# Kernel tuning notes

Measured on AMD Instinct MI355X. Metric: run time of the kernel, lower is better.

Reference implementation:

```python
import jax, jax.numpy as jnp
import numpy as np

PI_2 = 3.14159 / 2  # matches the torch module's pi_2 constant
EPS = 1e-8          # F.cosine_similarity default eps


def setup_inputs() -> dict:
    key = jax.random.key(0)
    k1, k2 = jax.random.split(key)
    B, N, C, H, W = 32, 2000, 512, 7, 7
    key_t = jax.random.normal(k1, (B, C, H, W), dtype=jnp.float32)
    memory = jax.random.normal(k2, (N, C, H, W), dtype=jnp.float32)
    return {"key": key_t, "memory": memory}


def reference(key, memory):
    # Memory.read(key): cosine-similarity addressing + tan warp + softmax, then weighted read.
    B = key.shape[0]
    N = memory.shape[0]
    k = key.reshape(B, -1)        # [B, D], D = C*H*W
    m = memory.reshape(N, -1)     # [N, D]
    # cosine similarity with torch's eps clamping on norms
    dots = jnp.einsum('bd,nd->bn', k, m)                                   # [B, N]
    k_norm = jnp.maximum(jnp.sqrt(jnp.sum(k * k, axis=-1, keepdims=True)), EPS)  # [B, 1]
    m_norm = jnp.maximum(jnp.sqrt(jnp.sum(m * m, axis=-1)), EPS)                 # [N]
    cos = dots / (k_norm * m_norm[None, :])                                 # [B, N]
    w = jax.nn.softmax(jnp.tan(cos * PI_2), axis=1)                         # [B, N]
    # weighted read: sum_n w[b,n] * memory[n,c,h,w] -> [B, C, H, W]
    out = jnp.einsum('bn,nchw->bchw', w, memory)
    return out
```

## Files before the change

### kernel.cpp

```cpp
#include <hip/hip_runtime.h>
#include <math.h>

#define D_ELEMS 25088
#define D4      6272
#define N_MEM   2000
#define B_KEYS  32
#define PI_2F   1.570795f
#define EPSF    1e-8f
#define NSLICE  49
#define KSLICE  512
#define KSTEPS  16
#define NWAVES  (125 * NSLICE)
#define RTILE   100

using short8 = __attribute__((ext_vector_type(8))) short;
using short4v = __attribute__((ext_vector_type(4))) short;
using f32x4  = __attribute__((ext_vector_type(4))) float;


__device__ inline short f2bf(float x) {
    union { float f; unsigned u; } v; v.f = x;
    unsigned r = v.u + 0x7fffu + ((v.u >> 16) & 1u);
    return (short)(r >> 16);
}

__global__ __launch_bounds__(256) void k_prep(const float* __restrict__ key,
                                              short* __restrict__ keyb) {
    const int i = blockIdx.x * 256 + threadIdx.x;
    const float4 f = ((const float4*)key)[i];
    short4v s; s[0] = f2bf(f.x); s[1] = f2bf(f.y); s[2] = f2bf(f.z); s[3] = f2bf(f.w);
    ((short4v*)keyb)[i] = s;
}

__global__ __launch_bounds__(256) void k_dots_mfma(const short* __restrict__ keyb,
                                                  const float* __restrict__ mem,
                                                  float* __restrict__ dots_part,
                                                  float* __restrict__ mn2_part) {
    const int wid = blockIdx.x * 4 + (threadIdx.x >> 6);
    if (wid >= NWAVES) return;
    const int nt   = wid / NSLICE;
    const int s    = wid % NSLICE;
    const int n0   = nt * 16;
    const int lane = threadIdx.x & 63;
    const int quad = lane >> 4;
    const int l16  = lane & 15;
    const int k0   = s * KSLICE + quad * 8;

    const short* a0p = keyb + (size_t)l16 * D_ELEMS + k0;
    const short* a1p = keyb + (size_t)(16 + l16) * D_ELEMS + k0;
    const float4* bp = (const float4*)(mem + (size_t)(n0 + l16) * D_ELEMS + k0);

    f32x4 acc0 = {0.f, 0.f, 0.f, 0.f};
    f32x4 acc1 = {0.f, 0.f, 0.f, 0.f};
    float msq = 0.f;

    short8 a0 = *(const short8*)a0p;
    short8 a1 = *(const short8*)a1p;
    float4 f0 = bp[0], f1 = bp[1];

    for (int t = 0; t < KSTEPS; ++t) {
        const short8 a0c = a0, a1c = a1;
        const float4 f0c = f0, f1c = f1;
        if (t + 1 < KSTEPS) {
            a0 = *(const short8*)(a0p + (t + 1) * 32);
            a1 = *(const short8*)(a1p + (t + 1) * 32);
            f0 = bp[(t + 1) * 8];
            f1 = bp[(t + 1) * 8 + 1];
        }
        msq += f0c.x * f0c.x + f0c.y * f0c.y + f0c.z * f0c.z + f0c.w * f0c.w
             + f1c.x * f1c.x + f1c.y * f1c.y + f1c.z * f1c.z + f1c.w * f1c.w;
        short8 b;
        b[0] = f2bf(f0c.x); b[1] = f2bf(f0c.y); b[2] = f2bf(f0c.z); b[3] = f2bf(f0c.w);
        b[4] = f2bf(f1c.x); b[5] = f2bf(f1c.y); b[6] = f2bf(f1c.z); b[7] = f2bf(f1c.w);
        acc0 = __builtin_amdgcn_mfma_f32_16x16x32_bf16(a0c, b, acc0, 0, 0, 0);
        acc1 = __builtin_amdgcn_mfma_f32_16x16x32_bf16(a1c, b, acc1, 0, 0, 0);
    }

    float* dp = dots_part + (size_t)(s * N_MEM + n0 + l16) * B_KEYS;
#pragma unroll
    for (int r = 0; r < 4; ++r) {
        dp[quad * 4 + r]      = acc0[r];
        dp[16 + quad * 4 + r] = acc1[r];
    }

    msq += __shfl_xor(msq, 16, 64);
    msq += __shfl_xor(msq, 32, 64);
    if (lane < 16) mn2_part[s * N_MEM + n0 + lane] = msq;
}

__global__ __launch_bounds__(256) void k_reduce(const float* __restrict__ dots_part,
                                                const float* __restrict__ mn2_part,
                                                float* __restrict__ dots,
                                                float* __restrict__ mn2) {
    const int gid = blockIdx.x * 256 + threadIdx.x;
    float ds = 0.f;
#pragma unroll
    for (int s = 0; s < NSLICE; ++s) ds += dots_part[s * (N_MEM * B_KEYS) + gid];
    dots[gid] = ds;
    if (gid < N_MEM) {
        float ms = 0.f;
#pragma unroll
        for (int s = 0; s < NSLICE; ++s) ms += mn2_part[s * N_MEM + gid];
        mn2[gid] = ms;
    }
}

__global__ __launch_bounds__(512) void k_softmax(const float* __restrict__ key,
                                                 const float* __restrict__ dots,
                                                 const float* __restrict__ mn2,
                                                 float* __restrict__ w) {
    const int b   = blockIdx.x;
    const int tid = threadIdx.x;
    __shared__ float sred[512];
    __shared__ float xbuf[N_MEM];

    const float4* K4 = (const float4*)(key + (size_t)b * D_ELEMS);
    float ks = 0.f;
    for (int i = tid; i < D4; i += 512) {
        const float4 kf = K4[i];
        ks += kf.x * kf.x + kf.y * kf.y + kf.z * kf.z + kf.w * kf.w;
    }
    sred[tid] = ks;
    __syncthreads();
    for (int o = 256; o; o >>= 1) {
        if (tid < o) sred[tid] += sred[tid + o];
        __syncthreads();
    }
    const float knorm = fmaxf(sqrtf(sred[0]), EPSF);
    __syncthreads();

    float mx = -1e30f;
    for (int n = tid; n < N_MEM; n += 512) {
        const float mn = fmaxf(sqrtf(mn2[n]), EPSF);
        const float x  = __tanf((dots[n * B_KEYS + b] / (knorm * mn)) * PI_2F);
        xbuf[n] = x;
        mx = fmaxf(mx, x);
    }
    sred[tid] = mx;
    __syncthreads();
    for (int o = 256; o; o >>= 1) {
        if (tid < o) sred[tid] = fmaxf(sred[tid], sred[tid + o]);
        __syncthreads();
    }
    mx = sred[0];
    __syncthreads();

    float sm = 0.f;
    for (int n = tid; n < N_MEM; n += 512) {
        const float e = __expf(xbuf[n] - mx);
        xbuf[n] = e;
        sm += e;
    }
    sred[tid] = sm;
    __syncthreads();
    for (int o = 256; o; o >>= 1) {
        if (tid < o) sred[tid] += sred[tid + o];
        __syncthreads();
    }
    const float inv = 1.f / sred[0];

    for (int n = tid; n < N_MEM; n += 512)
        w[n * B_KEYS + b] = xbuf[n] * inv;
}

__global__ __launch_bounds__(128, 2) void k_read(const float* __restrict__ mem,
                                                 const float* __restrict__ w,
                                                 float* __restrict__ partial,
                                                 int nPerS) {
    const int db  = blockIdx.x % 49;
    const int s   = blockIdx.x / 49;
    const int n0  = s * nPerS;
    const int tid = threadIdx.x;
    const int d4  = db * 128 + tid;

    const float4* M4 = (const float4*)mem;
    const float4* W4 = (const float4*)w;
    __shared__ float4 wls[RTILE * 8];

    float acc[32][4];
#pragma unroll
    for (int i = 0; i < 32; ++i) {
        acc[i][0] = 0.f; acc[i][1] = 0.f; acc[i][2] = 0.f; acc[i][3] = 0.f;
    }

    for (int c0 = 0; c0 < nPerS; c0 += RTILE) {
        __syncthreads();
        for (int i = tid; i < RTILE * 8; i += 128)
            wls[i] = W4[(size_t)(n0 + c0) * 8 + i];
        __syncthreads();

        const float4* mp = M4 + (size_t)(n0 + c0) * D4 + d4;
#pragma unroll 4
        for (int nn = 0; nn < RTILE; ++nn) {
            const float4 mc = mp[(size_t)nn * D4];
#pragma unroll
            for (int q = 0; q < 8; ++q) {
                const float4 wq = wls[nn * 8 + q];
                const int b0 = q * 4;
                acc[b0+0][0] += wq.x * mc.x; acc[b0+0][1] += wq.x * mc.y;
                acc[b0+0][2] += wq.x * mc.z; acc[b0+0][3] += wq.x * mc.w;
                acc[b0+1][0] += wq.y * mc.x; acc[b0+1][1] += wq.y * mc.y;
                acc[b0+1][2] += wq.y * mc.z; acc[b0+1][3] += wq.y * mc.w;
                acc[b0+2][0] += wq.z * mc.x; acc[b0+2][1] += wq.z * mc.y;
                acc[b0+2][2] += wq.z * mc.z; acc[b0+2][3] += wq.z * mc.w;
                acc[b0+3][0] += wq.w * mc.x; acc[b0+3][1] += wq.w * mc.y;
                acc[b0+3][2] += wq.w * mc.z; acc[b0+3][3] += wq.w * mc.w;
            }
        }
    }

    float4* P4 = (float4*)partial;
#pragma unroll
    for (int b = 0; b < 32; ++b)
        P4[(size_t)(s * B_KEYS + b) * D4 + d4] =
            make_float4(acc[b][0], acc[b][1], acc[b][2], acc[b][3]);
}

__global__ __launch_bounds__(256) void k_finish(const float* __restrict__ partial,
                                                float* __restrict__ out, int ns) {
    const int i = blockIdx.x * 256 + threadIdx.x;
    const float4* P4 = (const float4*)partial;
    float4 sum = P4[i];
    for (int s = 1; s < ns; ++s) {
        const float4 p = P4[(size_t)s * (B_KEYS * D4) + i];
        sum.x += p.x; sum.y += p.y; sum.z += p.z; sum.w += p.w;
    }
    ((float4*)out)[i] = sum;
}

extern "C" void kernel_launch(void* const* d_in, const int* in_sizes, int n_in,
                              void* d_out, int out_size, void* d_ws, size_t ws_size,
                              hipStream_t stream) {
    (void)in_sizes; (void)n_in; (void)out_size;
    const float* key = (const float*)d_in[0];
    const float* mem = (const float*)d_in[1];
    float* out = (float*)d_out;
    float* ws  = (float*)d_ws;

    short* keyb      = (short*)ws;
    float* dots_part = ws + 401408;
    float* mn2_part  = ws + 3537408;
    float* dots      = ws + 3635408;
    float* mn2       = ws + 3699408;
    float* w         = ws + 3701440;
    float* part      = ws + 3765440;

    int ns = 20;
    while (ns > 1 && (size_t)(3765440 + (size_t)ns * 802816) * 4 > ws_size)
        ns = (ns == 20) ? 10 : (ns == 10) ? 5 : (ns == 5) ? 2 : 1;
    const int nPerS = N_MEM / ns;

    k_prep     <<<784, 256, 0, stream>>>(key, keyb);
    k_dots_mfma<<<(NWAVES + 3) / 4, 256, 0, stream>>>(keyb, mem, dots_part, mn2_part);
    k_reduce   <<<250, 256, 0, stream>>>(dots_part, mn2_part, dots, mn2);
    k_softmax  <<<B_KEYS, 512, 0, stream>>>(key, dots, mn2, w);
    k_read     <<<49 * ns, 128, 0, stream>>>(mem, w, part, nPerS);
    k_finish   <<<784, 256, 0, stream>>>(part, out, ns);
}
```

Measured before the change: 392.1 us.

## Split k_read batch across waves and move key norm into separate kernel

k_read now uses 256-thread blocks in which pairs of waves share the same memory columns but each accumulates only 16 of the 32 keys. This halves the per-thread accumulator registers to raise occupancy and latency hiding, at the cost of each memory tile being loaded twice per block. The key-norm reduction is moved out of the 32-block softmax kernel into its own small kernel that uses wave shuffles, which shortens the serial softmax path but adds one launch.

```diff
diff --git a/kernel.cpp b/kernel.cpp
--- a/kernel.cpp
+++ b/kernel.cpp
@@ -30,6 +30,25 @@
     const float4 f = ((const float4*)key)[i];
     short4v s; s[0] = f2bf(f.x); s[1] = f2bf(f.y); s[2] = f2bf(f.z); s[3] = f2bf(f.w);
     ((short4v*)keyb)[i] = s;
+}
+
+__global__ __launch_bounds__(256) void k_knorm(const float* __restrict__ key,
+                                               float* __restrict__ knorm) {
+    const int b   = blockIdx.x;
+    const int tid = threadIdx.x;
+    const float4* K4 = (const float4*)(key + (size_t)b * D_ELEMS);
+    float ks = 0.f;
+    for (int i = tid; i < D4; i += 256) {
+        const float4 f = K4[i];
+        ks += f.x * f.x + f.y * f.y + f.z * f.z + f.w * f.w;
+    }
+#pragma unroll
+    for (int o = 1; o < 64; o <<= 1) ks += __shfl_xor(ks, o, 64);
+    __shared__ float sred[4];
+    if ((tid & 63) == 0) sred[tid >> 6] = ks;
+    __syncthreads();
+    if (tid == 0)
+        knorm[b] = fmaxf(sqrtf(sred[0] + sred[1] + sred[2] + sred[3]), EPSF);
 }
 
 __global__ __launch_bounds__(256) void k_dots_mfma(const short* __restrict__ keyb,
@@ -105,7 +124,7 @@
     }
 }
 
-__global__ __launch_bounds__(512) void k_softmax(const float* __restrict__ key,
+__global__ __launch_bounds__(512) void k_softmax(const float* __restrict__ knormArr,
                                                  const float* __restrict__ dots,
                                                  const float* __restrict__ mn2,
                                                  float* __restrict__ w) {
@@ -113,21 +132,7 @@
     const int tid = threadIdx.x;
     __shared__ float sred[512];
     __shared__ float xbuf[N_MEM];
-
-    const float4* K4 = (const float4*)(key + (size_t)b * D_ELEMS);
-    float ks = 0.f;
-    for (int i = tid; i < D4; i += 512) {
-        const float4 kf = K4[i];
-        ks += kf.x * kf.x + kf.y * kf.y + kf.z * kf.z + kf.w * kf.w;
-    }
-    sred[tid] = ks;
-    __syncthreads();
-    for (int o = 256; o; o >>= 1) {
-        if (tid < o) sred[tid] += sred[tid + o];
-        __syncthreads();
-    }
-    const float knorm = fmaxf(sqrtf(sred[0]), EPSF);
-    __syncthreads();
+    const float knorm = knormArr[b];
 
     float mx = -1e30f;
     for (int n = tid; n < N_MEM; n += 512) {
@@ -163,29 +168,32 @@
         w[n * B_KEYS + b] = xbuf[n] * inv;
 }
 
-__global__ __launch_bounds__(128, 2) void k_read(const float* __restrict__ mem,
+__global__ __launch_bounds__(256, 2) void k_read(const float* __restrict__ mem,
                                                  const float* __restrict__ w,
                                                  float* __restrict__ partial,
                                                  int nPerS) {
-    const int db  = blockIdx.x % 49;
-    const int s   = blockIdx.x / 49;
-    const int n0  = s * nPerS;
-    const int tid = threadIdx.x;
-    const int d4  = db * 128 + tid;
+    const int db   = blockIdx.x % 49;
+    const int s    = blockIdx.x / 49;
+    const int n0   = s * nPerS;
+    const int lane = threadIdx.x & 63;
+    const int wv   = threadIdx.x >> 6;
+    const int bh   = wv & 1;
+    const int dh   = wv >> 1;
+    const int d4   = db * 128 + dh * 64 + lane;
 
     const float4* M4 = (const float4*)mem;
     const float4* W4 = (const float4*)w;
     __shared__ float4 wls[RTILE * 8];
 
-    float acc[32][4];
-#pragma unroll
-    for (int i = 0; i < 32; ++i) {
+    float acc[16][4];
+#pragma unroll
+    for (int i = 0; i < 16; ++i) {
         acc[i][0] = 0.f; acc[i][1] = 0.f; acc[i][2] = 0.f; acc[i][3] = 0.f;
     }
 
     for (int c0 = 0; c0 < nPerS; c0 += RTILE) {
         __syncthreads();
-        for (int i = tid; i < RTILE * 8; i += 128)
+        for (int i = threadIdx.x; i < RTILE * 8; i += 256)
             wls[i] = W4[(size_t)(n0 + c0) * 8 + i];
         __syncthreads();
 
@@ -194,8 +202,8 @@
         for (int nn = 0; nn < RTILE; ++nn) {
             const float4 mc = mp[(size_t)nn * D4];
 #pragma unroll
-            for (int q = 0; q < 8; ++q) {
-                const float4 wq = wls[nn * 8 + q];
+            for (int q = 0; q < 4; ++q) {
+                const float4 wq = wls[nn * 8 + bh * 4 + q];
                 const int b0 = q * 4;
                 acc[b0+0][0] += wq.x * mc.x; acc[b0+0][1] += wq.x * mc.y;
                 acc[b0+0][2] += wq.x * mc.z; acc[b0+0][3] += wq.x * mc.w;
@@ -211,8 +219,8 @@
 
     float4* P4 = (float4*)partial;
 #pragma unroll
-    for (int b = 0; b < 32; ++b)
-        P4[(size_t)(s * B_KEYS + b) * D4 + d4] =
+    for (int b = 0; b < 16; ++b)
+        P4[(size_t)(s * B_KEYS + bh * 16 + b) * D4 + d4] =
             make_float4(acc[b][0], acc[b][1], acc[b][2], acc[b][3]);
 }
 
@@ -242,6 +250,7 @@
     float* mn2_part  = ws + 3537408;
     float* dots      = ws + 3635408;
     float* mn2       = ws + 3699408;
+    float* knorm     = ws + 3701408;
     float* w         = ws + 3701440;
     float* part      = ws + 3765440;
 
@@ -251,9 +260,10 @@
     const int nPerS = N_MEM / ns;
 
     k_prep     <<<784, 256, 0, stream>>>(key, keyb);
+    k_knorm    <<<B_KEYS, 256, 0, stream>>>(key, knorm);
     k_dots_mfma<<<(NWAVES + 3) / 4, 256, 0, stream>>>(keyb, mem, dots_part, mn2_part);
     k_reduce   <<<250, 256, 0, stream>>>(dots_part, mn2_part, dots, mn2);
-    k_softmax  <<<B_KEYS, 512, 0, stream>>>(key, dots, mn2, w);
-    k_read     <<<49 * ns, 128, 0, stream>>>(mem, w, part, nPerS);
+    k_softmax  <<<B_KEYS, 512, 0, stream>>>(knorm, dots, mn2, w);
+    k_read     <<<49 * ns, 256, 0, stream>>>(mem, w, part, nPerS);
     k_finish   <<<784, 256, 0, stream>>>(part, out, ns);
 }
```

New measurement: 377.3 us. 1.04x faster.
